# Kernel optimization log

Hardware: AMD Instinct MI355X
Metric: run time of the kernel (lower is better)

Reference implementation:

```python
import jax, jax.numpy as jnp
import numpy as np

B, C_IN, H, W = 32, 128, 64, 64
C_OUT, KH, KW = 256, 3, 3


def setup_inputs() -> dict:
    key = jax.random.key(0)
    k1, k2, k3 = jax.random.split(key, 3)
    inputs = jax.random.normal(k1, (B, C_IN, H, W), dtype=jnp.float32)
    weights = jax.random.normal(k2, (C_OUT, C_IN, KH, KW), dtype=jnp.float32) * 0.05
    bias = jax.random.normal(k3, (C_OUT, 1), dtype=jnp.float32)
    return {"inputs": inputs, "weights": weights, "bias": bias}


def reference(inputs, weights, bias):
    # Direct 2D valid convolution, stride 1, padding 0 (module default).
    # output[b,o,i,j] = sum_{c,u,v} inputs[b,c,i+u,j+v] * weights[o,c,u,v] + bias[o]
    out = jax.lax.conv_general_dilated(
        inputs, weights,
        window_strides=(1, 1),
        padding="VALID",
        dimension_numbers=("NCHW", "OIHW", "NCHW"),
    )
    # bias has shape (C_out, 1); broadcast per output channel
    return out + bias.reshape(1, -1, 1, 1)
```

## Files before the change

kernel.cpp:

```cpp
#include <hip/hip_runtime.h>
#include <hip/hip_bf16.h>
#include <stdint.h>

#define BB   32
#define CIN  128
#define HH   64
#define WW   64
#define COUT 256
#define OHH  62
#define OWW  62
#define PIX_PER_B (OHH*OWW)
#define NPIX (BB*PIX_PER_B)
#define KTOT (9*CIN)
#define NKT  18
#define SLOT_BYTES 49152

typedef __bf16 bf16x8 __attribute__((ext_vector_type(8)));
typedef float  f32x4  __attribute__((ext_vector_type(4)));
typedef uint16_t u16x8 __attribute__((ext_vector_type(8)));

__device__ __forceinline__ uint16_t f2bf(float f) {
    uint32_t u = __float_as_uint(f);
    uint32_t r = (u + 0x7FFFu + ((u >> 16) & 1u)) >> 16;
    return (uint16_t)r;
}

__device__ __forceinline__ void gload_lds16(const void* g, void* l) {
    __builtin_amdgcn_global_load_lds(
        (const __attribute__((address_space(1))) uint32_t*)g,
        (__attribute__((address_space(3))) uint32_t*)l, 16, 0, 0);
}

__global__ void __launch_bounds__(256) to_nhwc(const float* __restrict__ in,
                                               uint16_t* __restrict__ out) {
    int slab = blockIdx.x;
    int b = slab >> 6, h = slab & 63;
    int w  = threadIdx.x & 63;
    int cp = threadIdx.x >> 6;
    const float* src = in + (((size_t)b * CIN) * HH + h) * WW + w;
    uint16_t* dst = out + ((size_t)slab * WW + w) * CIN;
    #pragma unroll
    for (int it = 0; it < 4; ++it) {
        int c0 = cp * 32 + it * 8;
        u16x8 v;
        #pragma unroll
        for (int j = 0; j < 8; ++j) v[j] = f2bf(src[(c0 + j) * (HH * WW)]);
        *reinterpret_cast<u16x8*>(dst + c0) = v;
    }
}

__global__ void __launch_bounds__(256) pack_w(const float* __restrict__ w,
                                              uint16_t* __restrict__ out) {
    int idx = blockIdx.x * 256 + threadIdx.x;
    int o = idx / KTOT;
    int k = idx - o * KTOT;
    int uv = k >> 7, c = k & 127;
    out[idx] = f2bf(w[(o * CIN + c) * 9 + uv]);
}

__global__ void __launch_bounds__(512, 2) conv_mfma8(
        const uint16_t* __restrict__ Xg,
        const uint16_t* __restrict__ Wg,
        const float*    __restrict__ bias,
        float*          __restrict__ out)
{
    __shared__ char lds[3 * SLOT_BYTES + 1024];
    int* pbase = (int*)(lds + 3 * SLOT_BYTES);
    int* obase = pbase + 128;

    const int tid  = threadIdx.x;
    const int lane = tid & 63;
    const int wid  = tid >> 6;

    int bid = blockIdx.x;
    int xcd = bid & 7, lid = bid >> 3;
    int nt  = (xcd == 0 ? 0 : 121 + (xcd - 1) * 120) + lid;

    if (tid < 128) {
        int n   = nt * 128 + tid;
        int b   = n / PIX_PER_B;
        int rem = n - b * PIX_PER_B;
        int oh  = rem / OWW;
        int ow  = rem - oh * OWW;
        pbase[tid] = ((b * 64 + oh) * 64 + ow) * 128;
        obase[tid] = b * (COUT * PIX_PER_B) + rem;
    }
    __syncthreads();

    const int row8 = tid >> 3;
    const int ch   = tid & 7;
    const int kc   = ((ch ^ (row8 & 7)) << 4);
    const char* WgB = (const char*)Wg;
    const char* XgB = (const char*)Xg;
    int aoff[4], xoff[2];
    #pragma unroll
    for (int j = 0; j < 4; ++j) aoff[j] = (j * 64 + row8) * (KTOT * 2);
    #pragma unroll
    for (int j = 0; j < 2; ++j) xoff[j] = pbase[j * 64 + row8] * 2;
    const int ldst = tid * 16;

    auto stage_half = [&](int k, char* sbase, int h) {
        int uvv = k >> 1;
        int u   = uvv / 3, v = uvv - u * 3;
        int c0b = (k & 1) * 128;
        int wk  = uvv * 256 + c0b;
        int xk  = (u * 64 + v) * 256 + c0b;
        char* A = sbase;
        char* X = sbase + 32768;
        if (h == 0) {
            gload_lds16(WgB + (aoff[0] + wk + kc), A + 0 * 8192 + ldst);
            gload_lds16(WgB + (aoff[1] + wk + kc), A + 1 * 8192 + ldst);
            gload_lds16(XgB + (xoff[0] + xk + kc), X + 0 * 8192 + ldst);
        } else {
            gload_lds16(WgB + (aoff[2] + wk + kc), A + 2 * 8192 + ldst);
            gload_lds16(WgB + (aoff[3] + wk + kc), A + 3 * 8192 + ldst);
            gload_lds16(XgB + (xoff[1] + xk + kc), X + 1 * 8192 + ldst);
        }
    };

    const int wm = wid >> 1, wn = wid & 1;
    int aro[4][2], xro[4][2];
    #pragma unroll
    for (int mi = 0; mi < 4; ++mi) {
        int row = wm * 64 + mi * 16 + (lane & 15);
        #pragma unroll
        for (int ks = 0; ks < 2; ++ks)
            aro[mi][ks] = row * 128 +
                ((ks * 64 + (lane >> 4) * 16) ^ ((row & 7) << 4));
    }
    #pragma unroll
    for (int nj = 0; nj < 4; ++nj) {
        int row = wn * 64 + nj * 16 + (lane & 15);
        #pragma unroll
        for (int ks = 0; ks < 2; ++ks)
            xro[nj][ks] = 32768 + row * 128 +
                ((ks * 64 + (lane >> 4) * 16) ^ ((row & 7) << 4));
    }

    f32x4 acc[4][4] = {};

    stage_half(0, lds + 0 * SLOT_BYTES, 0);
    stage_half(0, lds + 0 * SLOT_BYTES, 1);
    stage_half(1, lds + 1 * SLOT_BYTES, 0);
    stage_half(1, lds + 1 * SLOT_BYTES, 1);
    asm volatile("s_waitcnt vmcnt(6)" ::: "memory");
    __builtin_amdgcn_s_barrier();

    int s = 0, s2 = 2;
    for (int kt = 0; kt < NKT; ++kt) {
        char* sb  = lds + s  * SLOT_BYTES;
        char* sb2 = lds + s2 * SLOT_BYTES;
        #pragma unroll
        for (int ks = 0; ks < 2; ++ks) {
            bf16x8 af[4], xf[4];
            #pragma unroll
            for (int mi = 0; mi < 4; ++mi)
                af[mi] = *reinterpret_cast<const bf16x8*>(sb + aro[mi][ks]);
            #pragma unroll
            for (int nj = 0; nj < 4; ++nj)
                xf[nj] = *reinterpret_cast<const bf16x8*>(sb + xro[nj][ks]);
            if (kt < NKT - 2) stage_half(kt + 2, sb2, ks);
            __builtin_amdgcn_s_barrier();
            __builtin_amdgcn_s_setprio(1);
            #pragma unroll
            for (int mi = 0; mi < 4; ++mi)
                #pragma unroll
                for (int nj = 0; nj < 4; ++nj)
                    acc[mi][nj] = __builtin_amdgcn_mfma_f32_16x16x32_bf16(
                        af[mi], xf[nj], acc[mi][nj], 0, 0, 0);
            __builtin_amdgcn_s_setprio(0);
            if (ks == 0) {
                __builtin_amdgcn_s_barrier();
            } else {
                if (kt < NKT - 2)
                    asm volatile("s_waitcnt vmcnt(6)" ::: "memory");
                else if (kt == NKT - 2)
                    asm volatile("s_waitcnt vmcnt(0)" ::: "memory");
                __builtin_amdgcn_s_barrier();
            }
        }
        s  = (s  == 2) ? 0 : s  + 1;
        s2 = (s2 == 2) ? 0 : s2 + 1;
    }

    #pragma unroll
    for (int mi = 0; mi < 4; ++mi) {
        int o = wm * 64 + mi * 16 + ((lane >> 4) << 2);
        #pragma unroll
        for (int reg = 0; reg < 4; ++reg) {
            float bv = bias[o + reg];
            #pragma unroll
            for (int nj = 0; nj < 4; ++nj) {
                int pl = wn * 64 + nj * 16 + (lane & 15);
                out[obase[pl] + (o + reg) * PIX_PER_B] = acc[mi][nj][reg] + bv;
            }
        }
    }
}

__global__ void __launch_bounds__(256) conv_naive(const float* __restrict__ in,
                                                  const float* __restrict__ w,
                                                  const float* __restrict__ bias,
                                                  float* __restrict__ out) {
    long idx = (long)blockIdx.x * 256 + threadIdx.x;
    int t = (int)idx;
    int ow = t % OWW; t /= OWW;
    int oh = t % OHH; t /= OHH;
    int o  = t % COUT;
    int b  = t / COUT;
    float s = bias[o];
    for (int c = 0; c < CIN; ++c)
        for (int u = 0; u < 3; ++u)
            for (int v = 0; v < 3; ++v)
                s += in[((b * CIN + c) * HH + oh + u) * WW + ow + v] *
                     w[((o * CIN + c) * 3 + u) * 3 + v];
    out[idx] = s;
}

extern "C" void kernel_launch(void* const* d_in, const int* in_sizes, int n_in,
                              void* d_out, int out_size, void* d_ws, size_t ws_size,
                              hipStream_t stream) {
    const float* in   = (const float*)d_in[0];
    const float* wt   = (const float*)d_in[1];
    const float* bias = (const float*)d_in[2];
    float* out = (float*)d_out;

    const size_t xg_elems = (size_t)BB * HH * WW * CIN;
    const size_t wg_elems = (size_t)COUT * KTOT;
    const size_t need = (xg_elems + wg_elems) * sizeof(uint16_t);

    if (ws_size < need) {
        long total = (long)BB * COUT * OHH * OWW;
        conv_naive<<<(int)((total + 255) / 256), 256, 0, stream>>>(in, wt, bias, out);
        return;
    }

    uint16_t* Xg = (uint16_t*)d_ws;
    uint16_t* Wg = Xg + xg_elems;

    to_nhwc<<<BB * HH, 256, 0, stream>>>(in, Xg);
    pack_w<<<(COUT * KTOT) / 256, 256, 0, stream>>>(wt, Wg);
    conv_mfma8<<<NPIX / 128, 512, 0, stream>>>(Xg, Wg, bias, out);
}
```

Baseline: 117.0 us.

## Halve K-tile per stage to shrink LDS and raise conv occupancy

Each pipeline stage of the MFMA conv GEMM now covers 32 K elements instead of 64, halving each LDS slot from 48KB to 24KB across the triple buffer. The aim is to let more blocks share a CU, so more waves are available to hide memory latency. The load swizzle is reworked to match the narrower 64-byte rows, and launch bounds now request 4 blocks. In exchange there are twice as many barriers and waits per K, and the tighter launch bound may cap VGPRs low enough to spill the 64-float accumulator.

```diff
diff --git a/kernel.cpp b/kernel.cpp
--- a/kernel.cpp
+++ b/kernel.cpp
@@ -12,8 +12,8 @@
 #define PIX_PER_B (OHH*OWW)
 #define NPIX (BB*PIX_PER_B)
 #define KTOT (9*CIN)
-#define NKT  18
-#define SLOT_BYTES 49152
+#define NKT  36
+#define SLOT 24576
 
 typedef __bf16 bf16x8 __attribute__((ext_vector_type(8)));
 typedef float  f32x4  __attribute__((ext_vector_type(4)));
@@ -58,14 +58,14 @@
     out[idx] = f2bf(w[(o * CIN + c) * 9 + uv]);
 }
 
-__global__ void __launch_bounds__(512, 2) conv_mfma8(
+__global__ void __launch_bounds__(512, 4) conv_k32(
         const uint16_t* __restrict__ Xg,
         const uint16_t* __restrict__ Wg,
         const float*    __restrict__ bias,
         float*          __restrict__ out)
 {
-    __shared__ char lds[3 * SLOT_BYTES + 1024];
-    int* pbase = (int*)(lds + 3 * SLOT_BYTES);
+    __shared__ char lds[3 * SLOT + 1024];
+    int* pbase = (int*)(lds + 3 * SLOT);
     int* obase = pbase + 128;
 
     const int tid  = threadIdx.x;
@@ -74,7 +74,7 @@
 
     int bid = blockIdx.x;
     int xcd = bid & 7, lid = bid >> 3;
-    int nt  = (xcd == 0 ? 0 : 121 + (xcd - 1) * 120) + lid;
+    int nt  = (xcd == 0 ? lid : 121 + (xcd - 1) * 120 + lid);
 
     if (tid < 128) {
         int n   = nt * 128 + tid;
@@ -87,98 +87,71 @@
     }
     __syncthreads();
 
-    const int row8 = tid >> 3;
-    const int ch   = tid & 7;
-    const int kc   = ((ch ^ (row8 & 7)) << 4);
+    const int cs   = (((tid & 3) ^ ((tid >> 3) & 3)) << 4);
+    const int ldst = tid * 16;
     const char* WgB = (const char*)Wg;
     const char* XgB = (const char*)Xg;
-    int aoff[4], xoff[2];
-    #pragma unroll
-    for (int j = 0; j < 4; ++j) aoff[j] = (j * 64 + row8) * (KTOT * 2);
-    #pragma unroll
-    for (int j = 0; j < 2; ++j) xoff[j] = pbase[j * 64 + row8] * 2;
-    const int ldst = tid * 16;
-
-    auto stage_half = [&](int k, char* sbase, int h) {
-        int uvv = k >> 1;
-        int u   = uvv / 3, v = uvv - u * 3;
-        int c0b = (k & 1) * 128;
-        int wk  = uvv * 256 + c0b;
-        int xk  = (u * 64 + v) * 256 + c0b;
-        char* A = sbase;
-        char* X = sbase + 32768;
-        if (h == 0) {
-            gload_lds16(WgB + (aoff[0] + wk + kc), A + 0 * 8192 + ldst);
-            gload_lds16(WgB + (aoff[1] + wk + kc), A + 1 * 8192 + ldst);
-            gload_lds16(XgB + (xoff[0] + xk + kc), X + 0 * 8192 + ldst);
-        } else {
-            gload_lds16(WgB + (aoff[2] + wk + kc), A + 2 * 8192 + ldst);
-            gload_lds16(WgB + (aoff[3] + wk + kc), A + 3 * 8192 + ldst);
-            gload_lds16(XgB + (xoff[1] + xk + kc), X + 1 * 8192 + ldst);
-        }
-    };
+    const int aow0 = (tid >> 2) * (KTOT * 2);
+    const int aow1 = (128 + (tid >> 2)) * (KTOT * 2);
+    const int pxw  = pbase[tid >> 2] * 2;
 
     const int wm = wid >> 1, wn = wid & 1;
-    int aro[4][2], xro[4][2];
+    int aro[4], xro[4];
     #pragma unroll
     for (int mi = 0; mi < 4; ++mi) {
         int row = wm * 64 + mi * 16 + (lane & 15);
-        #pragma unroll
-        for (int ks = 0; ks < 2; ++ks)
-            aro[mi][ks] = row * 128 +
-                ((ks * 64 + (lane >> 4) * 16) ^ ((row & 7) << 4));
+        aro[mi] = row * 64 + ((((lane >> 4) ^ ((row >> 1) & 3))) << 4);
     }
     #pragma unroll
     for (int nj = 0; nj < 4; ++nj) {
         int row = wn * 64 + nj * 16 + (lane & 15);
-        #pragma unroll
-        for (int ks = 0; ks < 2; ++ks)
-            xro[nj][ks] = 32768 + row * 128 +
-                ((ks * 64 + (lane >> 4) * 16) ^ ((row & 7) << 4));
+        xro[nj] = 16384 + row * 64 + ((((lane >> 4) ^ ((row >> 1) & 3))) << 4);
     }
 
     f32x4 acc[4][4] = {};
 
-    stage_half(0, lds + 0 * SLOT_BYTES, 0);
-    stage_half(0, lds + 0 * SLOT_BYTES, 1);
-    stage_half(1, lds + 1 * SLOT_BYTES, 0);
-    stage_half(1, lds + 1 * SLOT_BYTES, 1);
-    asm volatile("s_waitcnt vmcnt(6)" ::: "memory");
+    auto stage = [&](int t, char* dst) {
+        int uvv = t >> 2;
+        int u   = (uvv * 11) >> 5;
+        int v   = uvv - u * 3;
+        int kb  = ((t & 3) << 6) + cs;
+        gload_lds16(WgB + aow0 + uvv * 256 + kb, dst + ldst);
+        gload_lds16(WgB + aow1 + uvv * 256 + kb, dst + 8192 + ldst);
+        gload_lds16(XgB + pxw + (u * 64 + v) * 256 + kb, dst + 16384 + ldst);
+    };
+
+    stage(0, lds);
+    stage(1, lds + SLOT);
+    asm volatile("s_waitcnt vmcnt(3)" ::: "memory");
     __builtin_amdgcn_s_barrier();
 
     int s = 0, s2 = 2;
-    for (int kt = 0; kt < NKT; ++kt) {
-        char* sb  = lds + s  * SLOT_BYTES;
-        char* sb2 = lds + s2 * SLOT_BYTES;
-        #pragma unroll
-        for (int ks = 0; ks < 2; ++ks) {
-            bf16x8 af[4], xf[4];
-            #pragma unroll
-            for (int mi = 0; mi < 4; ++mi)
-                af[mi] = *reinterpret_cast<const bf16x8*>(sb + aro[mi][ks]);
+    for (int t = 0; t < NKT; ++t) {
+        char* slot = lds + s * SLOT;
+        bf16x8 af[4], xf[4];
+        #pragma unroll
+        for (int mi = 0; mi < 4; ++mi)
+            af[mi] = *reinterpret_cast<const bf16x8*>(slot + aro[mi]);
+        #pragma unroll
+        for (int nj = 0; nj < 4; ++nj)
+            xf[nj] = *reinterpret_cast<const bf16x8*>(slot + xro[nj]);
+        if (t + 2 < NKT) stage(t + 2, lds + s2 * SLOT);
+        __builtin_amdgcn_s_barrier();
+        asm volatile("s_waitcnt lgkmcnt(0)" ::: "memory");
+        __builtin_amdgcn_sched_barrier(0);
+        __builtin_amdgcn_s_setprio(1);
+        #pragma unroll
+        for (int mi = 0; mi < 4; ++mi)
             #pragma unroll
             for (int nj = 0; nj < 4; ++nj)
-                xf[nj] = *reinterpret_cast<const bf16x8*>(sb + xro[nj][ks]);
-            if (kt < NKT - 2) stage_half(kt + 2, sb2, ks);
-            __builtin_amdgcn_s_barrier();
-            __builtin_amdgcn_s_setprio(1);
-            #pragma unroll
-            for (int mi = 0; mi < 4; ++mi)
-                #pragma unroll
-                for (int nj = 0; nj < 4; ++nj)
-                    acc[mi][nj] = __builtin_amdgcn_mfma_f32_16x16x32_bf16(
-                        af[mi], xf[nj], acc[mi][nj], 0, 0, 0);
-            __builtin_amdgcn_s_setprio(0);
-            if (ks == 0) {
-                __builtin_amdgcn_s_barrier();
-            } else {
-                if (kt < NKT - 2)
-                    asm volatile("s_waitcnt vmcnt(6)" ::: "memory");
-                else if (kt == NKT - 2)
-                    asm volatile("s_waitcnt vmcnt(0)" ::: "memory");
-                __builtin_amdgcn_s_barrier();
-            }
-        }
+                acc[mi][nj] = __builtin_amdgcn_mfma_f32_16x16x32_bf16(
+                    af[mi], xf[nj], acc[mi][nj], 0, 0, 0);
+        __builtin_amdgcn_s_setprio(0);
+        if (t < NKT - 2)
+            asm volatile("s_waitcnt vmcnt(3)" ::: "memory");
+        else if (t == NKT - 2)
+            asm volatile("s_waitcnt vmcnt(0)" ::: "memory");
+        __builtin_amdgcn_s_barrier();
         s  = (s  == 2) ? 0 : s  + 1;
         s2 = (s2 == 2) ? 0 : s2 + 1;
     }
@@ -240,5 +213,5 @@
 
     to_nhwc<<<BB * HH, 256, 0, stream>>>(in, Xg);
     pack_w<<<(COUT * KTOT) / 256, 256, 0, stream>>>(wt, Wg);
-    conv_mfma8<<<NPIX / 128, 512, 0, stream>>>(Xg, Wg, bias, out);
-}
+    conv_k32<<<NPIX / 128, 512, 0, stream>>>(Xg, Wg, bias, out);
+}
```

New measurement: 109.6 us. -6.3%, faster.
